# Optimization experiments

Measured on AMD Instinct MI355X. Metric: run time of the kernel, lower is better.

Reference implementation:

```python
import jax, jax.numpy as jnp
import numpy as np

ALPHA = 100.0
EPS = 1e-12  # torch F.normalize eps


def setup_inputs() -> dict:
    key = jax.random.key(0)
    k1, k2 = jax.random.split(key)
    N, C, H, W, K = 32, 512, 56, 56, 64
    x = jax.random.normal(k1, (N, C, H, W), dtype=jnp.float32)
    centroids = jax.random.uniform(k2, (K, C), dtype=jnp.float32)  # torch.rand
    # _init_params: conv weight/bias are independent params initialized from centroids
    conv_w = 2.0 * ALPHA * centroids                      # (K, C), 1x1 conv kernel
    conv_b = -ALPHA * jnp.linalg.norm(centroids, axis=1)  # (K,)
    return {"x": x, "centroids": centroids, "conv_w": conv_w, "conv_b": conv_b}


def reference(x, centroids, conv_w, conv_b):
    N, C, H, W = x.shape
    K = centroids.shape[0]
    P = H * W
    xf = x.reshape(N, C, P)  # local descriptors, (N, C, P)

    # 1x1 conv == per-pixel linear; softmax over clusters
    logits = jnp.einsum('ncp,kc->nkp', xf, conv_w) + conv_b[None, :, None]
    a = jax.nn.softmax(logits, axis=1)  # (N, K, P)

    # Faithful to original: centroids.view(C, K) is a row-major RESHAPE, not transpose
    cent_r = jnp.reshape(centroids, (C, K))  # (C, K)

    # Algebraic rewrite of sum_p a[n,k,p] * (x[n,c,p] - cent_r[c,k]):
    # avoids the (N, C, K, P) intermediate entirely.
    vlad = jnp.einsum('ncp,nkp->nck', xf, a) - cent_r[None] * a.sum(-1)[:, None, :]  # (N, C, K)

    # intra-normalization over dim=2 (clusters), as in original code
    vlad = vlad / jnp.clip(jnp.linalg.norm(vlad, axis=2, keepdims=True), EPS)
    vlad = vlad.reshape(N, C * K)
    vlad = vlad / jnp.clip(jnp.linalg.norm(vlad, axis=1, keepdims=True), EPS)
    return vlad
```

## Files before the change

### kernel.cpp

```cpp
#include <hip/hip_runtime.h>
#include <math.h>

#define N_DIM 32
#define C_DIM 512
#define K_DIM 64
#define P_DIM 3136


__global__ __launch_bounds__(256) void k_prep(const float* __restrict__ conv_w,
                                              float* __restrict__ wt) {
    const int b = blockIdx.x, t = threadIdx.x;
#pragma unroll
    for (int r = 0; r < 4; ++r) {
        int idx = b * 1024 + r * 256 + t;
        int c = idx >> 6, k = idx & 63;
        wt[idx] = conv_w[k * C_DIM + c];
    }
}

__global__ __launch_bounds__(256) void k_logits(const float* __restrict__ x,
                                                const float* __restrict__ wt,
                                                const float* __restrict__ bias,
                                                float* __restrict__ a_t,
                                                float* __restrict__ asum_part) {
    __shared__ float xs[32][224];
    __shared__ float wsh[32][64];
    __shared__ float asl[4][64];
    const int tid = threadIdx.x;
    const int n  = blockIdx.y;
    const int pblk = blockIdx.x;
    const int p0 = pblk * 224;
    const int tp = tid >> 3;
    const int tk = tid & 7;

    float acc[7][8];
    {
        float4 b0 = *(const float4*)(bias + tk * 8);
        float4 b1 = *(const float4*)(bias + tk * 8 + 4);
        float br[8] = {b0.x, b0.y, b0.z, b0.w, b1.x, b1.y, b1.z, b1.w};
#pragma unroll
        for (int i = 0; i < 7; ++i)
#pragma unroll
            for (int j = 0; j < 8; ++j) acc[i][j] = br[j];
    }

    const float* xn = x + (size_t)n * C_DIM * P_DIM + p0;

    float4 xv[7], wv[2];
#pragma unroll
    for (int i = 0; i < 7; ++i) {
        int f = tid + 256 * i;
        xv[i] = *(const float4*)(xn + (size_t)(f / 56) * P_DIM + (f % 56) * 4);
    }
    wv[0] = *(const float4*)(wt + (tid >> 4) * K_DIM + (tid & 15) * 4);
    wv[1] = *(const float4*)(wt + ((tid + 256) >> 4) * K_DIM + (tid & 15) * 4);

    for (int cc = 0; cc < C_DIM; cc += 32) {
        __syncthreads();
#pragma unroll
        for (int i = 0; i < 7; ++i) {
            int f = tid + 256 * i;
            *(float4*)&xs[f / 56][(f % 56) * 4] = xv[i];
        }
        *(float4*)&wsh[tid >> 4][(tid & 15) * 4] = wv[0];
        *(float4*)&wsh[(tid + 256) >> 4][(tid & 15) * 4] = wv[1];
        __syncthreads();

        if (cc + 32 < C_DIM) {
            const float* xc = xn + (size_t)(cc + 32) * P_DIM;
#pragma unroll
            for (int i = 0; i < 7; ++i) {
                int f = tid + 256 * i;
                xv[i] = *(const float4*)(xc + (size_t)(f / 56) * P_DIM + (f % 56) * 4);
            }
            const float* wc = wt + (cc + 32) * K_DIM;
            wv[0] = *(const float4*)(wc + (tid >> 4) * K_DIM + (tid & 15) * 4);
            wv[1] = *(const float4*)(wc + ((tid + 256) >> 4) * K_DIM + (tid & 15) * 4);
        }

#pragma unroll 8
        for (int c = 0; c < 32; ++c) {
            float xr[7];
#pragma unroll
            for (int i = 0; i < 7; ++i) xr[i] = xs[c][tp + 32 * i];
            float4 w0 = *(const float4*)&wsh[c][tk * 8];
            float4 w1 = *(const float4*)&wsh[c][tk * 8 + 4];
            float wr[8] = {w0.x, w0.y, w0.z, w0.w, w1.x, w1.y, w1.z, w1.w};
#pragma unroll
            for (int i = 0; i < 7; ++i)
#pragma unroll
                for (int j = 0; j < 8; ++j)
                    acc[i][j] = fmaf(xr[i], wr[j], acc[i][j]);
        }
    }

    float sk[8] = {0.f, 0.f, 0.f, 0.f, 0.f, 0.f, 0.f, 0.f};
#pragma unroll
    for (int i = 0; i < 7; ++i) {
        float m = acc[i][0];
#pragma unroll
        for (int j = 1; j < 8; ++j) m = fmaxf(m, acc[i][j]);
        m = fmaxf(m, __shfl_xor(m, 1));
        m = fmaxf(m, __shfl_xor(m, 2));
        m = fmaxf(m, __shfl_xor(m, 4));
        float e[8], s = 0.f;
#pragma unroll
        for (int j = 0; j < 8; ++j) { e[j] = __expf(acc[i][j] - m); s += e[j]; }
        s += __shfl_xor(s, 1);
        s += __shfl_xor(s, 2);
        s += __shfl_xor(s, 4);
        const float inv = 1.0f / s;
        float* ap = a_t + ((size_t)n * P_DIM + p0 + tp + 32 * i) * K_DIM + tk * 8;
        float4 o0, o1;
        o0.x = e[0] * inv; o0.y = e[1] * inv; o0.z = e[2] * inv; o0.w = e[3] * inv;
        o1.x = e[4] * inv; o1.y = e[5] * inv; o1.z = e[6] * inv; o1.w = e[7] * inv;
        *(float4*)ap = o0;
        *(float4*)(ap + 4) = o1;
        sk[0] += o0.x; sk[1] += o0.y; sk[2] += o0.z; sk[3] += o0.w;
        sk[4] += o1.x; sk[5] += o1.y; sk[6] += o1.z; sk[7] += o1.w;
    }
#pragma unroll
    for (int j = 0; j < 8; ++j) {
        sk[j] += __shfl_xor(sk[j], 8);
        sk[j] += __shfl_xor(sk[j], 16);
        sk[j] += __shfl_xor(sk[j], 32);
    }
    const int lane = tid & 63, wv_ = tid >> 6;
    if (lane < 8) {
#pragma unroll
        for (int j = 0; j < 8; ++j) asl[wv_][lane * 8 + j] = sk[j];
    }
    __syncthreads();
    if (tid < 64)
        asum_part[((size_t)n * 14 + pblk) * K_DIM + tid] =
            asl[0][tid] + asl[1][tid] + asl[2][tid] + asl[3][tid];
}

__global__ __launch_bounds__(256) void k_red(const float* __restrict__ asum_part,
                                             float* __restrict__ asum) {
    const int idx = blockIdx.x * 256 + threadIdx.x;
    const int n = idx >> 6, k = idx & 63;
    float s = 0.f;
#pragma unroll
    for (int b = 0; b < 14; ++b)
        s += asum_part[((size_t)n * 14 + b) * K_DIM + k];
    asum[idx] = s;
}

__global__ __launch_bounds__(128) void k_gemm2(const float* __restrict__ x,
                                               const float* __restrict__ a_t,
                                               float* __restrict__ part,
                                               int pslice) {
    __shared__ float xs[16][132];
    __shared__ float as[16][64];
    const int tid = threadIdx.x;
    const int c0 = blockIdx.x * 128;
    const int n  = blockIdx.y;
    const int s  = blockIdx.z;
    const int p0 = s * pslice;
    const int tc = tid >> 3;
    const int tk = tid & 7;

    float acc[8][8];
#pragma unroll
    for (int i = 0; i < 8; ++i)
#pragma unroll
        for (int j = 0; j < 8; ++j) acc[i][j] = 0.f;

    const float* xb = x + ((size_t)n * C_DIM + c0) * P_DIM + p0;
    const float* ab = a_t + ((size_t)n * P_DIM + p0) * K_DIM;

    float4 xv[4], av[2];
#pragma unroll
    for (int i = 0; i < 4; ++i) {
        int f = tid + 128 * i;
        xv[i] = *(const float4*)(xb + (size_t)(f >> 2) * P_DIM + (f & 3) * 4);
    }
#pragma unroll
    for (int i = 0; i < 2; ++i) {
        int f = tid + 128 * i;
        av[i] = *(const float4*)(ab + (size_t)(f >> 4) * K_DIM + (f & 15) * 4);
    }

    for (int pb = 0; pb < pslice; pb += 16) {
        __syncthreads();
#pragma unroll
        for (int i = 0; i < 4; ++i) {
            int f = tid + 128 * i;
            int c = f >> 2, pe = (f & 3) * 4;
            xs[pe + 0][c] = xv[i].x;
            xs[pe + 1][c] = xv[i].y;
            xs[pe + 2][c] = xv[i].z;
            xs[pe + 3][c] = xv[i].w;
        }
#pragma unroll
        for (int i = 0; i < 2; ++i) {
            int f = tid + 128 * i;
            *(float4*)&as[f >> 4][(f & 15) * 4] = av[i];
        }
        __syncthreads();

        if (pb + 16 < pslice) {
            const float* xc = xb + pb + 16;
            const float* ac = ab + (size_t)(pb + 16) * K_DIM;
#pragma unroll
            for (int i = 0; i < 4; ++i) {
                int f = tid + 128 * i;
                xv[i] = *(const float4*)(xc + (size_t)(f >> 2) * P_DIM + (f & 3) * 4);
            }
#pragma unroll
            for (int i = 0; i < 2; ++i) {
                int f = tid + 128 * i;
                av[i] = *(const float4*)(ac + (size_t)(f >> 4) * K_DIM + (f & 15) * 4);
            }
        }

#pragma unroll 4
        for (int p = 0; p < 16; ++p) {
            float4 x0 = *(const float4*)&xs[p][tc * 8];
            float4 x1 = *(const float4*)&xs[p][tc * 8 + 4];
            float4 a0 = *(const float4*)&as[p][tk * 8];
            float4 a1 = *(const float4*)&as[p][tk * 8 + 4];
            float xr[8] = {x0.x, x0.y, x0.z, x0.w, x1.x, x1.y, x1.z, x1.w};
            float ar[8] = {a0.x, a0.y, a0.z, a0.w, a1.x, a1.y, a1.z, a1.w};
#pragma unroll
            for (int i = 0; i < 8; ++i)
#pragma unroll
                for (int j = 0; j < 8; ++j)
                    acc[i][j] = fmaf(xr[i], ar[j], acc[i][j]);
        }
    }

    float* po = part + (((size_t)s * N_DIM + n) * C_DIM + c0 + tc * 8) * K_DIM + tk * 8;
#pragma unroll
    for (int i = 0; i < 8; ++i) {
        float4 o0, o1;
        o0.x = acc[i][0]; o0.y = acc[i][1]; o0.z = acc[i][2]; o0.w = acc[i][3];
        o1.x = acc[i][4]; o1.y = acc[i][5]; o1.z = acc[i][6]; o1.w = acc[i][7];
        *(float4*)&po[(size_t)i * K_DIM] = o0;
        *(float4*)&po[(size_t)i * K_DIM + 4] = o1;
    }
}

template <int S>
__global__ __launch_bounds__(256) void k_intra(const float* __restrict__ part,
                                               const float* __restrict__ cent,
                                               const float* __restrict__ asum,
                                               float* __restrict__ out,
                                               float* __restrict__ ssb) {
    const int w = (blockIdx.x * 256 + threadIdx.x) >> 6;
    const int lane = threadIdx.x & 63;
    const int n = w >> 9;
    const int c = w & 511;
    const size_t off = ((size_t)n * C_DIM + c) * K_DIM + lane;
    const size_t stride = (size_t)N_DIM * C_DIM * K_DIM;

    float v = 0.f;
#pragma unroll
    for (int s = 0; s < S; ++s) v += part[s * stride + off];
    v -= cent[c * K_DIM + lane] * asum[n * K_DIM + lane];

    float ss = v * v;
#pragma unroll
    for (int o = 32; o > 0; o >>= 1) ss += __shfl_xor(ss, o);

    const float denom = fmaxf(sqrtf(ss), 1e-12f);
    out[off] = v / denom;
    if (lane == 0) ssb[w] = ss / (denom * denom);
}

__global__ __launch_bounds__(256) void k_gsum(const float* __restrict__ ssb,
                                              float* __restrict__ gsum) {
    const int n = blockIdx.x, t = threadIdx.x;
    float s = ssb[n * C_DIM + t] + ssb[n * C_DIM + t + 256];
    __shared__ float red[256];
    red[t] = s;
    __syncthreads();
    for (int o = 128; o > 0; o >>= 1) {
        if (t < o) red[t] += red[t + o];
        __syncthreads();
    }
    if (t == 0) gsum[n] = red[0];
}

__global__ __launch_bounds__(256) void k_final(float* __restrict__ out,
                                               const float* __restrict__ gsum) {
    const size_t i = (size_t)blockIdx.x * 256 + threadIdx.x;
    const int n = (int)(i >> 15);
    const float g = sqrtf(gsum[n]);
    out[i] = out[i] / fmaxf(g, 1e-12f);
}

extern "C" void kernel_launch(void* const* d_in, const int* in_sizes, int n_in,
                              void* d_out, int out_size, void* d_ws, size_t ws_size,
                              hipStream_t stream) {
    const float* x      = (const float*)d_in[0];
    const float* cent   = (const float*)d_in[1];
    const float* conv_w = (const float*)d_in[2];
    const float* conv_b = (const float*)d_in[3];

    float* ws    = (float*)d_ws;
    float* wt    = ws;
    float* a_t   = wt + 32768;
    float* asum  = a_t + (size_t)N_DIM * P_DIM * K_DIM;
    float* apart = asum + 2048;
    float* gsum  = apart + 28672;
    float* ssb   = gsum + 32;
    float* part  = ssb + 16384;
    float* out   = (float*)d_out;

    const size_t base_f = (size_t)(part - ws);
    const size_t cxk = (size_t)N_DIM * C_DIM * K_DIM;
    int S = 14;
    if (ws_size < (base_f + 14 * cxk) * 4) S = 7;
    if (ws_size < (base_f + 7 * cxk) * 4) S = 2;
    const int pslice = P_DIM / S;

    hipLaunchKernelGGL(k_prep,   dim3(32),        dim3(256), 0, stream, conv_w, wt);
    hipLaunchKernelGGL(k_logits, dim3(14, 32),    dim3(256), 0, stream, x, wt, conv_b, a_t, apart);
    hipLaunchKernelGGL(k_red,    dim3(8),         dim3(256), 0, stream, apart, asum);
    hipLaunchKernelGGL(k_gemm2,  dim3(4, 32, S),  dim3(128), 0, stream, x, a_t, part, pslice);
    if (S == 14)
        hipLaunchKernelGGL(k_intra<14>, dim3(4096), dim3(256), 0, stream, part, cent, asum, out, ssb);
    else if (S == 7)
        hipLaunchKernelGGL(k_intra<7>,  dim3(4096), dim3(256), 0, stream, part, cent, asum, out, ssb);
    else
        hipLaunchKernelGGL(k_intra<2>,  dim3(4096), dim3(256), 0, stream, part, cent, asum, out, ssb);
    hipLaunchKernelGGL(k_gsum,   dim3(32),        dim3(256), 0, stream, ssb, gsum);
    hipLaunchKernelGGL(k_final,  dim3(4096),      dim3(256), 0, stream, out, gsum);
}
```

Before: 507.3 us.

## Double logits kernel threads to 512 and halve per-thread cluster tile

The logits GEMM+softmax kernel now runs 512 threads per block, each computing 7 pixels by 4 clusters instead of 7 by 8. The channel chunk staged in LDS also doubles from 32 to 64. The softmax reductions gain an extra shuffle stage, and the cluster-sum reduction is spread over 8 waves. The aim is more waves per block to hide latency with fewer accumulator registers per thread, at the cost of lower per-thread register reuse, more LDS reads per FMA, and larger shared memory per block (about 74 KB).

```diff
diff --git a/kernel.cpp b/kernel.cpp
--- a/kernel.cpp
+++ b/kernel.cpp
@@ -18,30 +18,29 @@
     }
 }
 
-__global__ __launch_bounds__(256) void k_logits(const float* __restrict__ x,
+__global__ __launch_bounds__(512) void k_logits(const float* __restrict__ x,
                                                 const float* __restrict__ wt,
                                                 const float* __restrict__ bias,
                                                 float* __restrict__ a_t,
                                                 float* __restrict__ asum_part) {
-    __shared__ float xs[32][224];
-    __shared__ float wsh[32][64];
-    __shared__ float asl[4][64];
+    __shared__ float xs[64][224];
+    __shared__ float wsh[64][64];
+    __shared__ float asl[8][64];
     const int tid = threadIdx.x;
     const int n  = blockIdx.y;
     const int pblk = blockIdx.x;
     const int p0 = pblk * 224;
-    const int tp = tid >> 3;
-    const int tk = tid & 7;
-
-    float acc[7][8];
+    const int tp = tid >> 4;
+    const int tk = tid & 15;
+
+    float acc[7][4];
     {
-        float4 b0 = *(const float4*)(bias + tk * 8);
-        float4 b1 = *(const float4*)(bias + tk * 8 + 4);
-        float br[8] = {b0.x, b0.y, b0.z, b0.w, b1.x, b1.y, b1.z, b1.w};
+        float4 b0 = *(const float4*)(bias + tk * 4);
+        float br[4] = {b0.x, b0.y, b0.z, b0.w};
 #pragma unroll
         for (int i = 0; i < 7; ++i)
 #pragma unroll
-            for (int j = 0; j < 8; ++j) acc[i][j] = br[j];
+            for (int j = 0; j < 4; ++j) acc[i][j] = br[j];
     }
 
     const float* xn = x + (size_t)n * C_DIM * P_DIM + p0;
@@ -49,91 +48,100 @@
     float4 xv[7], wv[2];
 #pragma unroll
     for (int i = 0; i < 7; ++i) {
-        int f = tid + 256 * i;
+        int f = tid + 512 * i;
         xv[i] = *(const float4*)(xn + (size_t)(f / 56) * P_DIM + (f % 56) * 4);
     }
-    wv[0] = *(const float4*)(wt + (tid >> 4) * K_DIM + (tid & 15) * 4);
-    wv[1] = *(const float4*)(wt + ((tid + 256) >> 4) * K_DIM + (tid & 15) * 4);
-
-    for (int cc = 0; cc < C_DIM; cc += 32) {
+#pragma unroll
+    for (int i = 0; i < 2; ++i) {
+        int f = tid + 512 * i;
+        wv[i] = *(const float4*)(wt + (f >> 4) * K_DIM + (f & 15) * 4);
+    }
+
+    for (int cc = 0; cc < C_DIM; cc += 64) {
         __syncthreads();
 #pragma unroll
         for (int i = 0; i < 7; ++i) {
-            int f = tid + 256 * i;
+            int f = tid + 512 * i;
             *(float4*)&xs[f / 56][(f % 56) * 4] = xv[i];
         }
-        *(float4*)&wsh[tid >> 4][(tid & 15) * 4] = wv[0];
-        *(float4*)&wsh[(tid + 256) >> 4][(tid & 15) * 4] = wv[1];
-        __syncthreads();
-
-        if (cc + 32 < C_DIM) {
-            const float* xc = xn + (size_t)(cc + 32) * P_DIM;
+#pragma unroll
+        for (int i = 0; i < 2; ++i) {
+            int f = tid + 512 * i;
+            *(float4*)&wsh[f >> 4][(f & 15) * 4] = wv[i];
+        }
+        __syncthreads();
+
+        if (cc + 64 < C_DIM) {
+            const float* xc = xn + (size_t)(cc + 64) * P_DIM;
 #pragma unroll
             for (int i = 0; i < 7; ++i) {
-                int f = tid + 256 * i;
+                int f = tid + 512 * i;
                 xv[i] = *(const float4*)(xc + (size_t)(f / 56) * P_DIM + (f % 56) * 4);
             }
-            const float* wc = wt + (cc + 32) * K_DIM;
-            wv[0] = *(const float4*)(wc + (tid >> 4) * K_DIM + (tid & 15) * 4);
-            wv[1] = *(const float4*)(wc + ((tid + 256) >> 4) * K_DIM + (tid & 15) * 4);
+            const float* wc = wt + (cc + 64) * K_DIM;
+#pragma unroll
+            for (int i = 0; i < 2; ++i) {
+                int f = tid + 512 * i;
+                wv[i] = *(const float4*)(wc + (f >> 4) * K_DIM + (f & 15) * 4);
+            }
         }
 
 #pragma unroll 8
-        for (int c = 0; c < 32; ++c) {
+        for (int c = 0; c < 64; ++c) {
             float xr[7];
 #pragma unroll
             for (int i = 0; i < 7; ++i) xr[i] = xs[c][tp + 32 * i];
-            float4 w0 = *(const float4*)&wsh[c][tk * 8];
-            float4 w1 = *(const float4*)&wsh[c][tk * 8 + 4];
-            float wr[8] = {w0.x, w0.y, w0.z, w0.w, w1.x, w1.y, w1.z, w1.w};
+            float4 w0 = *(const float4*)&wsh[c][tk * 4];
+            float wr[4] = {w0.x, w0.y, w0.z, w0.w};
 #pragma unroll
             for (int i = 0; i < 7; ++i)
 #pragma unroll
-                for (int j = 0; j < 8; ++j)
+                for (int j = 0; j < 4; ++j)
                     acc[i][j] = fmaf(xr[i], wr[j], acc[i][j]);
         }
     }
 
-    float sk[8] = {0.f, 0.f, 0.f, 0.f, 0.f, 0.f, 0.f, 0.f};
+    float sk[4] = {0.f, 0.f, 0.f, 0.f};
 #pragma unroll
     for (int i = 0; i < 7; ++i) {
-        float m = acc[i][0];
-#pragma unroll
-        for (int j = 1; j < 8; ++j) m = fmaxf(m, acc[i][j]);
+        float m = fmaxf(fmaxf(acc[i][0], acc[i][1]), fmaxf(acc[i][2], acc[i][3]));
         m = fmaxf(m, __shfl_xor(m, 1));
         m = fmaxf(m, __shfl_xor(m, 2));
         m = fmaxf(m, __shfl_xor(m, 4));
-        float e[8], s = 0.f;
-#pragma unroll
-        for (int j = 0; j < 8; ++j) { e[j] = __expf(acc[i][j] - m); s += e[j]; }
+        m = fmaxf(m, __shfl_xor(m, 8));
+        float e0 = __expf(acc[i][0] - m);
+        float e1 = __expf(acc[i][1] - m);
+        float e2 = __expf(acc[i][2] - m);
+        float e3 = __expf(acc[i][3] - m);
+        float s = (e0 + e1) + (e2 + e3);
         s += __shfl_xor(s, 1);
         s += __shfl_xor(s, 2);
         s += __shfl_xor(s, 4);
+        s += __shfl_xor(s, 8);
         const float inv = 1.0f / s;
-        float* ap = a_t + ((size_t)n * P_DIM + p0 + tp + 32 * i) * K_DIM + tk * 8;
-        float4 o0, o1;
-        o0.x = e[0] * inv; o0.y = e[1] * inv; o0.z = e[2] * inv; o0.w = e[3] * inv;
-        o1.x = e[4] * inv; o1.y = e[5] * inv; o1.z = e[6] * inv; o1.w = e[7] * inv;
-        *(float4*)ap = o0;
-        *(float4*)(ap + 4) = o1;
-        sk[0] += o0.x; sk[1] += o0.y; sk[2] += o0.z; sk[3] += o0.w;
-        sk[4] += o1.x; sk[5] += o1.y; sk[6] += o1.z; sk[7] += o1.w;
-    }
-#pragma unroll
-    for (int j = 0; j < 8; ++j) {
-        sk[j] += __shfl_xor(sk[j], 8);
+        float4 o;
+        o.x = e0 * inv; o.y = e1 * inv; o.z = e2 * inv; o.w = e3 * inv;
+        float* ap = a_t + ((size_t)n * P_DIM + p0 + tp + 32 * i) * K_DIM + tk * 4;
+        *(float4*)ap = o;
+        sk[0] += o.x; sk[1] += o.y; sk[2] += o.z; sk[3] += o.w;
+    }
+#pragma unroll
+    for (int j = 0; j < 4; ++j) {
         sk[j] += __shfl_xor(sk[j], 16);
         sk[j] += __shfl_xor(sk[j], 32);
     }
-    const int lane = tid & 63, wv_ = tid >> 6;
-    if (lane < 8) {
-#pragma unroll
-        for (int j = 0; j < 8; ++j) asl[wv_][lane * 8 + j] = sk[j];
+    const int lane = tid & 63, wid = tid >> 6;
+    if (lane < 16) {
+#pragma unroll
+        for (int j = 0; j < 4; ++j) asl[wid][lane * 4 + j] = sk[j];
     }
     __syncthreads();
-    if (tid < 64)
-        asum_part[((size_t)n * 14 + pblk) * K_DIM + tid] =
-            asl[0][tid] + asl[1][tid] + asl[2][tid] + asl[3][tid];
+    if (tid < 64) {
+        float s = 0.f;
+#pragma unroll
+        for (int w = 0; w < 8; ++w) s += asl[w][tid];
+        asum_part[((size_t)n * 14 + pblk) * K_DIM + tid] = s;
+    }
 }
 
 __global__ __launch_bounds__(256) void k_red(const float* __restrict__ asum_part,
@@ -317,7 +325,7 @@
     const int pslice = P_DIM / S;
 
     hipLaunchKernelGGL(k_prep,   dim3(32),        dim3(256), 0, stream, conv_w, wt);
-    hipLaunchKernelGGL(k_logits, dim3(14, 32),    dim3(256), 0, stream, x, wt, conv_b, a_t, apart);
+    hipLaunchKernelGGL(k_logits, dim3(14, 32),    dim3(512), 0, stream, x, wt, conv_b, a_t, apart);
     hipLaunchKernelGGL(k_red,    dim3(8),         dim3(256), 0, stream, apart, asum);
     hipLaunchKernelGGL(k_gemm2,  dim3(4, 32, S),  dim3(128), 0, stream, x, a_t, part, pslice);
     if (S == 14)
```

After: 523.1 us. 3.1% more time.

## Replace shared-memory tiled logits GEMM with register-direct loads and smaller blocks

Applied to the files above, without the earlier changes.

Rewrites the logits/softmax kernel to drop the LDS staging of x and weights. Each thread now loads float4 slices of x (4 consecutive pixels) and its 8 weights directly from global memory, with a 4-deep register prefetch. Blocks shrink to 128 threads covering 64 pixels, so the grid grows from 14 to 49 blocks per image, and the partial-sum buffer and reduction are resized to match. This removes the barriers and LDS traffic and raises the block count for occupancy. In exchange the weights are re-read from global/L1 by every thread with no shared reuse, and each thread computes a smaller 4x8 tile.

```diff
diff --git a/kernel.cpp b/kernel.cpp
--- a/kernel.cpp
+++ b/kernel.cpp
@@ -5,6 +5,7 @@
 #define C_DIM 512
 #define K_DIM 64
 #define P_DIM 3136
+#define ABLK 49
 
 
 __global__ __launch_bounds__(256) void k_prep(const float* __restrict__ conv_w,
@@ -18,85 +19,65 @@
     }
 }
 
-__global__ __launch_bounds__(256) void k_logits(const float* __restrict__ x,
+__global__ __launch_bounds__(128) void k_logits(const float* __restrict__ x,
                                                 const float* __restrict__ wt,
                                                 const float* __restrict__ bias,
                                                 float* __restrict__ a_t,
                                                 float* __restrict__ asum_part) {
-    __shared__ float xs[32][224];
-    __shared__ float wsh[32][64];
-    __shared__ float asl[4][64];
+    __shared__ float asl[2][64];
     const int tid = threadIdx.x;
-    const int n  = blockIdx.y;
+    const int n    = blockIdx.y;
     const int pblk = blockIdx.x;
-    const int p0 = pblk * 224;
+    const int tk = tid & 7;
     const int tp = tid >> 3;
-    const int tk = tid & 7;
-
-    float acc[7][8];
+    const int p0 = pblk * 64 + tp * 4;
+
+    float acc[4][8];
     {
         float4 b0 = *(const float4*)(bias + tk * 8);
         float4 b1 = *(const float4*)(bias + tk * 8 + 4);
         float br[8] = {b0.x, b0.y, b0.z, b0.w, b1.x, b1.y, b1.z, b1.w};
 #pragma unroll
-        for (int i = 0; i < 7; ++i)
+        for (int i = 0; i < 4; ++i)
 #pragma unroll
             for (int j = 0; j < 8; ++j) acc[i][j] = br[j];
     }
 
-    const float* xn = x + (size_t)n * C_DIM * P_DIM + p0;
-
-    float4 xv[7], wv[2];
-#pragma unroll
-    for (int i = 0; i < 7; ++i) {
-        int f = tid + 256 * i;
-        xv[i] = *(const float4*)(xn + (size_t)(f / 56) * P_DIM + (f % 56) * 4);
-    }
-    wv[0] = *(const float4*)(wt + (tid >> 4) * K_DIM + (tid & 15) * 4);
-    wv[1] = *(const float4*)(wt + ((tid + 256) >> 4) * K_DIM + (tid & 15) * 4);
-
-    for (int cc = 0; cc < C_DIM; cc += 32) {
-        __syncthreads();
-#pragma unroll
-        for (int i = 0; i < 7; ++i) {
-            int f = tid + 256 * i;
-            *(float4*)&xs[f / 56][(f % 56) * 4] = xv[i];
-        }
-        *(float4*)&wsh[tid >> 4][(tid & 15) * 4] = wv[0];
-        *(float4*)&wsh[(tid + 256) >> 4][(tid & 15) * 4] = wv[1];
-        __syncthreads();
-
-        if (cc + 32 < C_DIM) {
-            const float* xc = xn + (size_t)(cc + 32) * P_DIM;
-#pragma unroll
-            for (int i = 0; i < 7; ++i) {
-                int f = tid + 256 * i;
-                xv[i] = *(const float4*)(xc + (size_t)(f / 56) * P_DIM + (f % 56) * 4);
+    const float* xp = x + (size_t)n * C_DIM * P_DIM + p0;
+    const float* wp = wt + tk * 8;
+
+    float4 xb[4], wa[4], wb[4];
+#pragma unroll
+    for (int d = 0; d < 4; ++d) {
+        xb[d] = *(const float4*)(xp + (size_t)d * P_DIM);
+        wa[d] = *(const float4*)(wp + d * K_DIM);
+        wb[d] = *(const float4*)(wp + d * K_DIM + 4);
+    }
+
+    for (int c = 0; c < C_DIM; c += 4) {
+#pragma unroll
+        for (int u = 0; u < 4; ++u) {
+            float xr[4] = {xb[u].x, xb[u].y, xb[u].z, xb[u].w};
+            float wr[8] = {wa[u].x, wa[u].y, wa[u].z, wa[u].w,
+                           wb[u].x, wb[u].y, wb[u].z, wb[u].w};
+            if (c + 4 + u < C_DIM) {
+                xb[u] = *(const float4*)(xp + (size_t)(4 + u) * P_DIM);
+                wa[u] = *(const float4*)(wp + (4 + u) * K_DIM);
+                wb[u] = *(const float4*)(wp + (4 + u) * K_DIM + 4);
             }
-            const float* wc = wt + (cc + 32) * K_DIM;
-            wv[0] = *(const float4*)(wc + (tid >> 4) * K_DIM + (tid & 15) * 4);
-            wv[1] = *(const float4*)(wc + ((tid + 256) >> 4) * K_DIM + (tid & 15) * 4);
-        }
-
-#pragma unroll 8
-        for (int c = 0; c < 32; ++c) {
-            float xr[7];
-#pragma unroll
-            for (int i = 0; i < 7; ++i) xr[i] = xs[c][tp + 32 * i];
-            float4 w0 = *(const float4*)&wsh[c][tk * 8];
-            float4 w1 = *(const float4*)&wsh[c][tk * 8 + 4];
-            float wr[8] = {w0.x, w0.y, w0.z, w0.w, w1.x, w1.y, w1.z, w1.w};
-#pragma unroll
-            for (int i = 0; i < 7; ++i)
+#pragma unroll
+            for (int i = 0; i < 4; ++i)
 #pragma unroll
                 for (int j = 0; j < 8; ++j)
                     acc[i][j] = fmaf(xr[i], wr[j], acc[i][j]);
         }
+        xp += (size_t)4 * P_DIM;
+        wp += 4 * K_DIM;
     }
 
     float sk[8] = {0.f, 0.f, 0.f, 0.f, 0.f, 0.f, 0.f, 0.f};
 #pragma unroll
-    for (int i = 0; i < 7; ++i) {
+    for (int i = 0; i < 4; ++i) {
         float m = acc[i][0];
 #pragma unroll
         for (int j = 1; j < 8; ++j) m = fmaxf(m, acc[i][j]);
@@ -110,10 +91,10 @@
         s += __shfl_xor(s, 2);
         s += __shfl_xor(s, 4);
         const float inv = 1.0f / s;
-        float* ap = a_t + ((size_t)n * P_DIM + p0 + tp + 32 * i) * K_DIM + tk * 8;
         float4 o0, o1;
         o0.x = e[0] * inv; o0.y = e[1] * inv; o0.z = e[2] * inv; o0.w = e[3] * inv;
         o1.x = e[4] * inv; o1.y = e[5] * inv; o1.z = e[6] * inv; o1.w = e[7] * inv;
+        float* ap = a_t + ((size_t)n * P_DIM + p0 + i) * K_DIM + tk * 8;
         *(float4*)ap = o0;
         *(float4*)(ap + 4) = o1;
         sk[0] += o0.x; sk[1] += o0.y; sk[2] += o0.z; sk[3] += o0.w;
@@ -125,15 +106,14 @@
         sk[j] += __shfl_xor(sk[j], 16);
         sk[j] += __shfl_xor(sk[j], 32);
     }
-    const int lane = tid & 63, wv_ = tid >> 6;
+    const int lane = tid & 63, wid = tid >> 6;
     if (lane < 8) {
 #pragma unroll
-        for (int j = 0; j < 8; ++j) asl[wv_][lane * 8 + j] = sk[j];
+        for (int j = 0; j < 8; ++j) asl[wid][lane * 8 + j] = sk[j];
     }
     __syncthreads();
     if (tid < 64)
-        asum_part[((size_t)n * 14 + pblk) * K_DIM + tid] =
-            asl[0][tid] + asl[1][tid] + asl[2][tid] + asl[3][tid];
+        asum_part[((size_t)n * ABLK + pblk) * K_DIM + tid] = asl[0][tid] + asl[1][tid];
 }
 
 __global__ __launch_bounds__(256) void k_red(const float* __restrict__ asum_part,
@@ -142,8 +122,8 @@
     const int n = idx >> 6, k = idx & 63;
     float s = 0.f;
 #pragma unroll
-    for (int b = 0; b < 14; ++b)
-        s += asum_part[((size_t)n * 14 + b) * K_DIM + k];
+    for (int b = 0; b < ABLK; ++b)
+        s += asum_part[((size_t)n * ABLK + b) * K_DIM + k];
     asum[idx] = s;
 }
 
@@ -304,7 +284,7 @@
     float* a_t   = wt + 32768;
     float* asum  = a_t + (size_t)N_DIM * P_DIM * K_DIM;
     float* apart = asum + 2048;
-    float* gsum  = apart + 28672;
+    float* gsum  = apart + (size_t)N_DIM * ABLK * K_DIM;
     float* ssb   = gsum + 32;
     float* part  = ssb + 16384;
     float* out   = (float*)d_out;
@@ -317,7 +297,7 @@
     const int pslice = P_DIM / S;
 
     hipLaunchKernelGGL(k_prep,   dim3(32),        dim3(256), 0, stream, conv_w, wt);
-    hipLaunchKernelGGL(k_logits, dim3(14, 32),    dim3(256), 0, stream, x, wt, conv_b, a_t, apart);
+    hipLaunchKernelGGL(k_logits, dim3(ABLK, 32),  dim3(128), 0, stream, x, wt, conv_b, a_t, apart);
     hipLaunchKernelGGL(k_red,    dim3(8),         dim3(256), 0, stream, apart, asum);
     hipLaunchKernelGGL(k_gemm2,  dim3(4, 32, S),  dim3(128), 0, stream, x, a_t, part, pslice);
     if (S == 14)
```

After: 735.0 us. +44.9%, slower.
